# Kernel tuning notes

Hardware: AMD Instinct MI355X
Metric: run time of the kernel (lower is better)

Reference implementation:

```python
import jax, jax.numpy as jnp
import numpy as np

B, T, WSZ, HS = 32768, 168, 4, 1  # batch, seq (one week of hours), weather dims, HIDDEN_DIM


def _uniform(key, shape, lim):
    return jax.random.uniform(key, shape, jnp.float32, -lim, lim)


def setup_inputs() -> dict:
    key = jax.random.key(0)
    ks = jax.random.split(key, 12)
    stdv = 1.0 / np.sqrt(HS)  # pew_LSTM init: uniform(-1/sqrt(H), 1/sqrt(H))
    xav = np.sqrt(6.0 / (HS + 1))  # xavier_uniform for fc (in=HS, out=1)
    return {
        "input": jax.random.normal(ks[0], (B, T, WSZ + 1), dtype=jnp.float32),
        # pew_LSTM layer 1 (input_sz=1)
        "W1_ih": _uniform(ks[1], (1, 4 * HS), stdv),
        "W1_hh": _uniform(ks[2], (HS, 4 * HS), stdv),
        "W1_wh": _uniform(ks[3], (WSZ, 4 * HS), stdv),
        "b1": _uniform(ks[4], (4 * HS,), stdv),
        # pew_LSTM layer 2 (input_sz=HS)
        "W2_ih": _uniform(ks[5], (HS, 4 * HS), stdv),
        "W2_hh": _uniform(ks[6], (HS, 4 * HS), stdv),
        "W2_wh": _uniform(ks[7], (WSZ, 4 * HS), stdv),
        "b2": _uniform(ks[8], (4 * HS,), stdv),
        # final Linear(HS, 1)
        "fc_w": _uniform(ks[9], (1, HS), xav),
        "fc_b": jnp.zeros((1,), jnp.float32),
    }


def _pew_lstm(x, w, Wih, Whh, Wwh, b):
    """Custom LSTM with per-step weather input added to the gate pre-activations.
    x: [B,T,D_in], w: [B,T,WSZ] -> hidden_seq [B,T,HS], c_T [B,HS]."""
    bs = x.shape[0]
    h0 = jnp.zeros((bs, HS), x.dtype)
    c0 = jnp.zeros((bs, HS), x.dtype)
    # input- and weather-dependent gate terms are time-parallel; precompute once
    g_pre = jnp.einsum('btd,dg->btg', x, Wih) + jnp.einsum('btw,wg->btg', w, Wwh) + b

    def step(carry, gp_t):
        h, c = carry
        gates = gp_t + h @ Whh  # [B, 4*HS]
        i = jax.nn.sigmoid(gates[:, 0 * HS:1 * HS])
        f = jax.nn.sigmoid(gates[:, 1 * HS:2 * HS])
        g = jnp.tanh(gates[:, 2 * HS:3 * HS])
        o = jax.nn.sigmoid(gates[:, 3 * HS:4 * HS])
        c = f * c + i * g
        h = o * jnp.tanh(c)
        return (h, c), h

    (_, cT), hs = jax.lax.scan(step, (h0, c0), jnp.swapaxes(g_pre, 0, 1))
    return jnp.swapaxes(hs, 0, 1), cT  # [B,T,HS], [B,HS]


def reference(input, W1_ih, W1_hh, W1_wh, b1, W2_ih, W2_hh, W2_wh, b2, fc_w, fc_b):
    x_weather = input[:, :, :-1]            # [B,T,4]
    x_input = input[:, :, -1:]              # [B,T,1]
    h1, _ = _pew_lstm(x_input, x_weather, W1_ih, W1_hh, W1_wh, b1)
    h2, _ = _pew_lstm(h1, x_weather, W2_ih, W2_hh, W2_wh, b2)
    out = h2.reshape(-1, HS) @ fc_w.T + fc_b  # [B*T, 1]
    return out.reshape(-1)                    # [B*T]
```

## Files before the change

kernel.cpp:

```cpp
#include <hip/hip_runtime.h>


constexpr int BB  = 32768;
constexpr int TT  = 168;
constexpr int CHS = 8;
constexpr int CHV = 10;
constexpr int NCH = 21;

#define LOG2E  1.44269504088896341f
#define NEG2L  (-2.88539008177792681f)
#define ACLAMP 40.0f

__device__ __forceinline__ float lane_swap(float x) {
    return __int_as_float(
        __builtin_amdgcn_mov_dpp(__float_as_int(x), 0xB1, 0xF, 0xF, true));
}

__global__ __launch_bounds__(64, 1) void pewlstm_kernel(
    const float* __restrict__ in,
    const float* __restrict__ W1ih, const float* __restrict__ W1hh,
    const float* __restrict__ W1wh, const float* __restrict__ b1,
    const float* __restrict__ W2ih, const float* __restrict__ W2hh,
    const float* __restrict__ W2wh, const float* __restrict__ b2,
    const float* __restrict__ fcw, const float* __restrict__ fcb,
    float* __restrict__ out)
{
    const int tid = blockIdx.x * 64 + threadIdx.x;
    const int b   = tid >> 1;
    const int l2  = tid & 1;
    const float l2f = l2 ? 1.0f : 0.0f;

    const float* Wih = l2 ? W2ih : W1ih;
    const float* Whh = l2 ? W2hh : W1hh;
    const float* Wwh = l2 ? W2wh : W1wh;
    const float* Bv  = l2 ? b2   : b1;

    float wih[4], whh[4], bbv[4], wwh[16];
#pragma unroll
    for (int g = 0; g < 4; ++g) {
        const float s = (g == 2) ? NEG2L : -LOG2E;
        wih[g] = Wih[g] * s; whh[g] = Whh[g] * s; bbv[g] = Bv[g] * s;
    }
#pragma unroll
    for (int k = 0; k < 16; ++k) {
        const float s = ((k & 3) == 2) ? NEG2L : -LOG2E;
        wwh[k] = Wwh[k] * s;
    }
    const float fw = fcw[0], fbv = fcb[0];

    const float4* __restrict__ row =
        reinterpret_cast<const float4*>(in + (size_t)b * (TT * 5));
    float4* orow = reinterpret_cast<float4*>(out + (size_t)b * TT);

    float4 pref[CHV];
#pragma unroll
    for (int i = 0; i < CHV; ++i) pref[i] = row[i];

    float h = 0.f, cc = 0.f, h1x = 0.f;
    float xc0 = 0.f, xc1 = 0.f, xc2 = 0.f, xc3 = 0.f;
    float ob[CHS];
    float preA[CHS][4], preB[CHS][4];
    float cur[CHS * 5];

    auto commit = [&]() {
#pragma unroll
        for (int i = 0; i < CHV; ++i) {
            float4 v = pref[i];
            cur[4*i+0] = v.x; cur[4*i+1] = v.y;
            cur[4*i+2] = v.z; cur[4*i+3] = v.w;
        }
    };
    auto issue = [&](int c2) {
        const float4* nr = row + c2 * CHV;
#pragma unroll
        for (int i = 0; i < CHV; ++i) pref[i] = nr[i];
    };

    auto run_chunk = [&](float (&pC)[CHS][4], float (&pN)[CHS][4],
                         int c, bool buildNext) {
        const bool is0 = (c == 0);
#pragma unroll
        for (int s = 0; s < CHS; ++s) {
            if (buildNext) {
                const float w0 = l2 ? (s == 0 ? xc0 : cur[(s-1)*5+0]) : cur[s*5+0];
                const float w1 = l2 ? (s == 0 ? xc1 : cur[(s-1)*5+1]) : cur[s*5+1];
                const float w2 = l2 ? (s == 0 ? xc2 : cur[(s-1)*5+2]) : cur[s*5+2];
                const float w3 = l2 ? (s == 0 ? xc3 : cur[(s-1)*5+3]) : cur[s*5+3];
                const float xi = l2 ? 0.0f : cur[s*5+4];
#pragma unroll
                for (int g = 0; g < 4; ++g) {
                    float p = bbv[g];
                    p = fmaf(w0, wwh[0  + g], p);
                    p = fmaf(w1, wwh[4  + g], p);
                    p = fmaf(w2, wwh[8  + g], p);
                    p = fmaf(w3, wwh[12 + g], p);
                    pN[s][g] = fmaf(xi, wih[g], p);
                }
            }
            const float inv = h1x * l2f;
            float a0 = fmaf(h, whh[0], fmaf(inv, wih[0], pC[s][0]));
            float a1 = fmaf(h, whh[1], fmaf(inv, wih[1], pC[s][1]));
            float a2 = fmaf(h, whh[2], fmaf(inv, wih[2], pC[s][2]));
            float a3 = fmaf(h, whh[3], fmaf(inv, wih[3], pC[s][3]));
            a0 = fminf(a0, ACLAMP); a1 = fminf(a1, ACLAMP);
            a2 = fminf(a2, ACLAMP); a3 = fminf(a3, ACLAMP);
            const float eI = __builtin_amdgcn_exp2f(a0);
            const float eF = __builtin_amdgcn_exp2f(a1);
            const float eG = __builtin_amdgcn_exp2f(a2);
            const float eO = __builtin_amdgcn_exp2f(a3);
            const float dI = 1.f + eI, dF = 1.f + eF;
            const float dG = 1.f + eG, dO = 1.f + eO;
            const float nG = 1.f - eG;
            const float p   = dI * dG;
            const float num = fmaf(cc, p, nG * dF);
            const float den = dF * p;
            cc = num * __builtin_amdgcn_rcpf(den);
            const float Cm = fminf(cc * NEG2L, ACLAMP);
            const float eC = __builtin_amdgcn_exp2f(Cm);
            const float dC = 1.f + eC, nC = 1.f - eC;
            h = nC * __builtin_amdgcn_rcpf(dO * dC);

            if (s == 0) { if (is0 && l2) { h = 0.f; cc = 0.f; } }

            ob[(s + CHS - 1) & (CHS - 1)] = fmaf(h, fw, fbv);

            if (s == 0 && l2 && c >= 1) {
                orow[(c-1)*2+0] = make_float4(ob[0], ob[1], ob[2], ob[3]);
                orow[(c-1)*2+1] = make_float4(ob[4], ob[5], ob[6], ob[7]);
            }

            h1x = lane_swap(h);
        }
        if (buildNext) {
            xc0 = cur[35]; xc1 = cur[36]; xc2 = cur[37]; xc3 = cur[38];
        }
    };

    commit();
#pragma unroll
    for (int s = 0; s < CHS; ++s) {
        const float w0 = l2 ? (s == 0 ? 0.f : cur[(s-1)*5+0]) : cur[s*5+0];
        const float w1 = l2 ? (s == 0 ? 0.f : cur[(s-1)*5+1]) : cur[s*5+1];
        const float w2 = l2 ? (s == 0 ? 0.f : cur[(s-1)*5+2]) : cur[s*5+2];
        const float w3 = l2 ? (s == 0 ? 0.f : cur[(s-1)*5+3]) : cur[s*5+3];
        const float xi = l2 ? 0.0f : cur[s*5+4];
#pragma unroll
        for (int g = 0; g < 4; ++g) {
            float pp = bbv[g];
            pp = fmaf(w0, wwh[0  + g], pp);
            pp = fmaf(w1, wwh[4  + g], pp);
            pp = fmaf(w2, wwh[8  + g], pp);
            pp = fmaf(w3, wwh[12 + g], pp);
            preA[s][g] = fmaf(xi, wih[g], pp);
        }
    }
    xc0 = cur[35]; xc1 = cur[36]; xc2 = cur[37]; xc3 = cur[38];
    issue(1);

    for (int cp = 0; cp < 10; ++cp) {
        const int c0 = 2 * cp;
        commit();
        if (c0 + 2 < NCH) issue(c0 + 2);
        run_chunk(preA, preB, c0, true);

        commit();
        if (c0 + 3 < NCH) issue(c0 + 3);
        run_chunk(preB, preA, c0 + 1, true);
    }

    run_chunk(preA, preB, NCH - 1, false);

    {
        float a[4];
#pragma unroll
        for (int g = 0; g < 4; ++g) {
            float pp = bbv[g];
            pp = fmaf(xc0, wwh[0  + g], pp);
            pp = fmaf(xc1, wwh[4  + g], pp);
            pp = fmaf(xc2, wwh[8  + g], pp);
            pp = fmaf(xc3, wwh[12 + g], pp);
            pp = fmaf(h1x, wih[g], pp);
            a[g] = fminf(fmaf(h, whh[g], pp), ACLAMP);
        }
        const float eI = __builtin_amdgcn_exp2f(a[0]);
        const float eF = __builtin_amdgcn_exp2f(a[1]);
        const float eG = __builtin_amdgcn_exp2f(a[2]);
        const float eO = __builtin_amdgcn_exp2f(a[3]);
        const float dI = 1.f + eI, dF = 1.f + eF;
        const float dG = 1.f + eG, dO = 1.f + eO;
        const float nG = 1.f - eG;
        const float p   = dI * dG;
        const float num = fmaf(cc, p, nG * dF);
        cc = num * __builtin_amdgcn_rcpf(dF * p);
        const float Cm = fminf(cc * NEG2L, ACLAMP);
        const float eC = __builtin_amdgcn_exp2f(Cm);
        h = (1.f - eC) * __builtin_amdgcn_rcpf(dO * (1.f + eC));
        ob[7] = fmaf(h, fw, fbv);
        if (l2) {
            orow[(NCH-1)*2+0] = make_float4(ob[0], ob[1], ob[2], ob[3]);
            orow[(NCH-1)*2+1] = make_float4(ob[4], ob[5], ob[6], ob[7]);
        }
    }
}

extern "C" void kernel_launch(void* const* d_in, const int* in_sizes, int n_in,
                              void* d_out, int out_size, void* d_ws, size_t ws_size,
                              hipStream_t stream) {
    const float* in   = (const float*)d_in[0];
    const float* W1ih = (const float*)d_in[1];
    const float* W1hh = (const float*)d_in[2];
    const float* W1wh = (const float*)d_in[3];
    const float* b1   = (const float*)d_in[4];
    const float* W2ih = (const float*)d_in[5];
    const float* W2hh = (const float*)d_in[6];
    const float* W2wh = (const float*)d_in[7];
    const float* b2   = (const float*)d_in[8];
    const float* fcw  = (const float*)d_in[9];
    const float* fcb  = (const float*)d_in[10];
    float* out = (float*)d_out;

    pewlstm_kernel<<<(BB * 2) / 64, 64, 0, stream>>>(
        in, W1ih, W1hh, W1wh, b1, W2ih, W2hh, W2wh, b2, fcw, fcb, out);
}
```

Measured before the change: 33.39 us.

## Split LSTM gates across lane pairs with DPP exchange, four lanes per batch row

Each batch row is now handled by four lanes instead of two: per layer, two lanes each compute two of the four gate pre-activations and exponentials, then exchange denominators through DPP moves. Hidden state is broadcast back with DPP so both lanes of a layer carry the same h and c. This halves the per-lane exp and FMA work on the serial recurrence chain and doubles the number of waves in flight, with launch bounds raised accordingly. In exchange each lane adds three DPP moves per step, and the weather stream is loaded redundantly by four lanes per row.

```diff
diff --git a/kernel.cpp b/kernel.cpp
--- a/kernel.cpp
+++ b/kernel.cpp
@@ -11,12 +11,17 @@
 #define NEG2L  (-2.88539008177792681f)
 #define ACLAMP 40.0f
 
-__device__ __forceinline__ float lane_swap(float x) {
-    return __int_as_float(
-        __builtin_amdgcn_mov_dpp(__float_as_int(x), 0xB1, 0xF, 0xF, true));
-}
-
-__global__ __launch_bounds__(64, 1) void pewlstm_kernel(
+__device__ __forceinline__ float dpp_pull(float x) {
+    return __int_as_float(__builtin_amdgcn_mov_dpp(__float_as_int(x), 0xB1, 0xF, 0xF, true));
+}
+__device__ __forceinline__ float dpp_bA(float x) {
+    return __int_as_float(__builtin_amdgcn_mov_dpp(__float_as_int(x), 0xA0, 0xF, 0xF, true));
+}
+__device__ __forceinline__ float dpp_b0(float x) {
+    return __int_as_float(__builtin_amdgcn_mov_dpp(__float_as_int(x), 0x00, 0xF, 0xF, true));
+}
+
+__global__ __launch_bounds__(64, 2) void pewlstm_kernel(
     const float* __restrict__ in,
     const float* __restrict__ W1ih, const float* __restrict__ W1hh,
     const float* __restrict__ W1wh, const float* __restrict__ b1,
@@ -26,8 +31,10 @@
     float* __restrict__ out)
 {
     const int tid = blockIdx.x * 64 + threadIdx.x;
-    const int b   = tid >> 1;
-    const int l2  = tid & 1;
+    const int q   = tid >> 2;
+    const int r   = tid & 3;
+    const int l2  = r >> 1;
+    const int go  = (r & 1) * 2;
     const float l2f = l2 ? 1.0f : 0.0f;
 
     const float* Wih = l2 ? W2ih : W1ih;
@@ -35,22 +42,22 @@
     const float* Wwh = l2 ? W2wh : W1wh;
     const float* Bv  = l2 ? b2   : b1;
 
-    float wih[4], whh[4], bbv[4], wwh[16];
-#pragma unroll
-    for (int g = 0; g < 4; ++g) {
-        const float s = (g == 2) ? NEG2L : -LOG2E;
-        wih[g] = Wih[g] * s; whh[g] = Whh[g] * s; bbv[g] = Bv[g] * s;
-    }
-#pragma unroll
-    for (int k = 0; k < 16; ++k) {
-        const float s = ((k & 3) == 2) ? NEG2L : -LOG2E;
-        wwh[k] = Wwh[k] * s;
+    const float sLo = (go == 2) ? NEG2L : -LOG2E;
+    const float sHi = -LOG2E;
+    const float wihLo = Wih[go] * sLo,  wihHi = Wih[go + 1] * sHi;
+    const float whhLo = Whh[go] * sLo,  whhHi = Whh[go + 1] * sHi;
+    const float bLo   = Bv[go]  * sLo,  bHi   = Bv[go + 1]  * sHi;
+    float wwLo[4], wwHi[4];
+#pragma unroll
+    for (int w = 0; w < 4; ++w) {
+        wwLo[w] = Wwh[w * 4 + go]     * sLo;
+        wwHi[w] = Wwh[w * 4 + go + 1] * sHi;
     }
     const float fw = fcw[0], fbv = fcb[0];
 
     const float4* __restrict__ row =
-        reinterpret_cast<const float4*>(in + (size_t)b * (TT * 5));
-    float4* orow = reinterpret_cast<float4*>(out + (size_t)b * TT);
+        reinterpret_cast<const float4*>(in + (size_t)q * (TT * 5));
+    float4* orow = reinterpret_cast<float4*>(out + (size_t)q * TT);
 
     float4 pref[CHV];
 #pragma unroll
@@ -59,7 +66,7 @@
     float h = 0.f, cc = 0.f, h1x = 0.f;
     float xc0 = 0.f, xc1 = 0.f, xc2 = 0.f, xc3 = 0.f;
     float ob[CHS];
-    float preA[CHS][4], preB[CHS][4];
+    float pLoA[CHS], pHiA[CHS], pLoB[CHS], pHiB[CHS];
     float cur[CHS * 5];
 
     auto commit = [&]() {
@@ -76,127 +83,106 @@
         for (int i = 0; i < CHV; ++i) pref[i] = nr[i];
     };
 
-    auto run_chunk = [&](float (&pC)[CHS][4], float (&pN)[CHS][4],
-                         int c, bool buildNext) {
-        const bool is0 = (c == 0);
+    auto build = [&](float (&pLo)[CHS], float (&pHi)[CHS]) {
 #pragma unroll
         for (int s = 0; s < CHS; ++s) {
-            if (buildNext) {
-                const float w0 = l2 ? (s == 0 ? xc0 : cur[(s-1)*5+0]) : cur[s*5+0];
-                const float w1 = l2 ? (s == 0 ? xc1 : cur[(s-1)*5+1]) : cur[s*5+1];
-                const float w2 = l2 ? (s == 0 ? xc2 : cur[(s-1)*5+2]) : cur[s*5+2];
-                const float w3 = l2 ? (s == 0 ? xc3 : cur[(s-1)*5+3]) : cur[s*5+3];
-                const float xi = l2 ? 0.0f : cur[s*5+4];
-#pragma unroll
-                for (int g = 0; g < 4; ++g) {
-                    float p = bbv[g];
-                    p = fmaf(w0, wwh[0  + g], p);
-                    p = fmaf(w1, wwh[4  + g], p);
-                    p = fmaf(w2, wwh[8  + g], p);
-                    p = fmaf(w3, wwh[12 + g], p);
-                    pN[s][g] = fmaf(xi, wih[g], p);
-                }
-            }
+            const float w0 = l2 ? (s == 0 ? xc0 : cur[(s-1)*5+0]) : cur[s*5+0];
+            const float w1 = l2 ? (s == 0 ? xc1 : cur[(s-1)*5+1]) : cur[s*5+1];
+            const float w2 = l2 ? (s == 0 ? xc2 : cur[(s-1)*5+2]) : cur[s*5+2];
+            const float w3 = l2 ? (s == 0 ? xc3 : cur[(s-1)*5+3]) : cur[s*5+3];
+            const float xi = l2 ? 0.0f : cur[s*5+4];
+            float a = bLo;
+            a = fmaf(w0, wwLo[0], a); a = fmaf(w1, wwLo[1], a);
+            a = fmaf(w2, wwLo[2], a); a = fmaf(w3, wwLo[3], a);
+            pLo[s] = fmaf(xi, wihLo, a);
+            float bb = bHi;
+            bb = fmaf(w0, wwHi[0], bb); bb = fmaf(w1, wwHi[1], bb);
+            bb = fmaf(w2, wwHi[2], bb); bb = fmaf(w3, wwHi[3], bb);
+            pHi[s] = fmaf(xi, wihHi, bb);
+        }
+        xc0 = cur[35]; xc1 = cur[36]; xc2 = cur[37]; xc3 = cur[38];
+    };
+
+    auto phase2 = [&](float (&pLo)[CHS], float (&pHi)[CHS], int c, bool is0) {
+#pragma unroll
+        for (int s = 0; s < CHS; ++s) {
             const float inv = h1x * l2f;
-            float a0 = fmaf(h, whh[0], fmaf(inv, wih[0], pC[s][0]));
-            float a1 = fmaf(h, whh[1], fmaf(inv, wih[1], pC[s][1]));
-            float a2 = fmaf(h, whh[2], fmaf(inv, wih[2], pC[s][2]));
-            float a3 = fmaf(h, whh[3], fmaf(inv, wih[3], pC[s][3]));
-            a0 = fminf(a0, ACLAMP); a1 = fminf(a1, ACLAMP);
-            a2 = fminf(a2, ACLAMP); a3 = fminf(a3, ACLAMP);
-            const float eI = __builtin_amdgcn_exp2f(a0);
-            const float eF = __builtin_amdgcn_exp2f(a1);
-            const float eG = __builtin_amdgcn_exp2f(a2);
-            const float eO = __builtin_amdgcn_exp2f(a3);
-            const float dI = 1.f + eI, dF = 1.f + eF;
-            const float dG = 1.f + eG, dO = 1.f + eO;
-            const float nG = 1.f - eG;
-            const float p   = dI * dG;
-            const float num = fmaf(cc, p, nG * dF);
-            const float den = dF * p;
+            float aLo = fmaf(h, whhLo, fmaf(inv, wihLo, pLo[s]));
+            float aHi = fmaf(h, whhHi, fmaf(inv, wihHi, pHi[s]));
+            aLo = fminf(aLo, ACLAMP); aHi = fminf(aHi, ACLAMP);
+            const float eLo = __builtin_amdgcn_exp2f(aLo);
+            const float eHi = __builtin_amdgcn_exp2f(aHi);
+            const float dLo = 1.f + eLo;
+            const float dHi = 1.f + eHi;
+            const float nLo = 1.f - eLo;
+            const float dG = dpp_pull(dLo);
+            const float nG = dpp_pull(nLo);
+            const float dO = dpp_pull(dHi);
+            const float p   = dLo * dG;
+            const float num = fmaf(cc, p, nG * dHi);
+            const float den = dHi * p;
             cc = num * __builtin_amdgcn_rcpf(den);
             const float Cm = fminf(cc * NEG2L, ACLAMP);
             const float eC = __builtin_amdgcn_exp2f(Cm);
-            const float dC = 1.f + eC, nC = 1.f - eC;
-            h = nC * __builtin_amdgcn_rcpf(dO * dC);
-
-            if (s == 0) { if (is0 && l2) { h = 0.f; cc = 0.f; } }
-
-            ob[(s + CHS - 1) & (CHS - 1)] = fmaf(h, fw, fbv);
-
-            if (s == 0 && l2 && c >= 1) {
+            h = (1.f - eC) * __builtin_amdgcn_rcpf(dO * (1.f + eC));
+
+            if (s == 0 && is0) { if (l2) { h = 0.f; cc = 0.f; } }
+
+            ob[(s + 7) & 7] = fmaf(h, fw, fbv);
+
+            if (s == 0 && c >= 1 && r == 2) {
                 orow[(c-1)*2+0] = make_float4(ob[0], ob[1], ob[2], ob[3]);
                 orow[(c-1)*2+1] = make_float4(ob[4], ob[5], ob[6], ob[7]);
             }
 
-            h1x = lane_swap(h);
-        }
-        if (buildNext) {
-            xc0 = cur[35]; xc1 = cur[36]; xc2 = cur[37]; xc3 = cur[38];
+            const float hb = h;
+            h1x = dpp_b0(hb);
+            h   = dpp_bA(hb);
         }
     };
 
     commit();
-#pragma unroll
-    for (int s = 0; s < CHS; ++s) {
-        const float w0 = l2 ? (s == 0 ? 0.f : cur[(s-1)*5+0]) : cur[s*5+0];
-        const float w1 = l2 ? (s == 0 ? 0.f : cur[(s-1)*5+1]) : cur[s*5+1];
-        const float w2 = l2 ? (s == 0 ? 0.f : cur[(s-1)*5+2]) : cur[s*5+2];
-        const float w3 = l2 ? (s == 0 ? 0.f : cur[(s-1)*5+3]) : cur[s*5+3];
-        const float xi = l2 ? 0.0f : cur[s*5+4];
-#pragma unroll
-        for (int g = 0; g < 4; ++g) {
-            float pp = bbv[g];
-            pp = fmaf(w0, wwh[0  + g], pp);
-            pp = fmaf(w1, wwh[4  + g], pp);
-            pp = fmaf(w2, wwh[8  + g], pp);
-            pp = fmaf(w3, wwh[12 + g], pp);
-            preA[s][g] = fmaf(xi, wih[g], pp);
-        }
-    }
-    xc0 = cur[35]; xc1 = cur[36]; xc2 = cur[37]; xc3 = cur[38];
+    build(pLoA, pHiA);
     issue(1);
 
     for (int cp = 0; cp < 10; ++cp) {
         const int c0 = 2 * cp;
         commit();
         if (c0 + 2 < NCH) issue(c0 + 2);
-        run_chunk(preA, preB, c0, true);
+        build(pLoB, pHiB);
+        phase2(pLoA, pHiA, c0, c0 == 0);
 
         commit();
         if (c0 + 3 < NCH) issue(c0 + 3);
-        run_chunk(preB, preA, c0 + 1, true);
+        build(pLoA, pHiA);
+        phase2(pLoB, pHiB, c0 + 1, false);
     }
 
-    run_chunk(preA, preB, NCH - 1, false);
+    phase2(pLoA, pHiA, NCH - 1, false);
 
     {
-        float a[4];
-#pragma unroll
-        for (int g = 0; g < 4; ++g) {
-            float pp = bbv[g];
-            pp = fmaf(xc0, wwh[0  + g], pp);
-            pp = fmaf(xc1, wwh[4  + g], pp);
-            pp = fmaf(xc2, wwh[8  + g], pp);
-            pp = fmaf(xc3, wwh[12 + g], pp);
-            pp = fmaf(h1x, wih[g], pp);
-            a[g] = fminf(fmaf(h, whh[g], pp), ACLAMP);
-        }
-        const float eI = __builtin_amdgcn_exp2f(a[0]);
-        const float eF = __builtin_amdgcn_exp2f(a[1]);
-        const float eG = __builtin_amdgcn_exp2f(a[2]);
-        const float eO = __builtin_amdgcn_exp2f(a[3]);
-        const float dI = 1.f + eI, dF = 1.f + eF;
-        const float dG = 1.f + eG, dO = 1.f + eO;
-        const float nG = 1.f - eG;
-        const float p   = dI * dG;
-        const float num = fmaf(cc, p, nG * dF);
-        cc = num * __builtin_amdgcn_rcpf(dF * p);
+        float aLo = bLo, aHi = bHi;
+        aLo = fmaf(xc0, wwLo[0], aLo); aHi = fmaf(xc0, wwHi[0], aHi);
+        aLo = fmaf(xc1, wwLo[1], aLo); aHi = fmaf(xc1, wwHi[1], aHi);
+        aLo = fmaf(xc2, wwLo[2], aLo); aHi = fmaf(xc2, wwHi[2], aHi);
+        aLo = fmaf(xc3, wwLo[3], aLo); aHi = fmaf(xc3, wwHi[3], aHi);
+        aLo = fmaf(h1x, wihLo, aLo);   aHi = fmaf(h1x, wihHi, aHi);
+        aLo = fmaf(h,   whhLo, aLo);   aHi = fmaf(h,   whhHi, aHi);
+        aLo = fminf(aLo, ACLAMP); aHi = fminf(aHi, ACLAMP);
+        const float eLo = __builtin_amdgcn_exp2f(aLo);
+        const float eHi = __builtin_amdgcn_exp2f(aHi);
+        const float dLo = 1.f + eLo, dHi = 1.f + eHi, nLo = 1.f - eLo;
+        const float dG = dpp_pull(dLo);
+        const float nG = dpp_pull(nLo);
+        const float dO = dpp_pull(dHi);
+        const float p   = dLo * dG;
+        const float num = fmaf(cc, p, nG * dHi);
+        cc = num * __builtin_amdgcn_rcpf(dHi * p);
         const float Cm = fminf(cc * NEG2L, ACLAMP);
         const float eC = __builtin_amdgcn_exp2f(Cm);
         h = (1.f - eC) * __builtin_amdgcn_rcpf(dO * (1.f + eC));
         ob[7] = fmaf(h, fw, fbv);
-        if (l2) {
+        if (r == 2) {
             orow[(NCH-1)*2+0] = make_float4(ob[0], ob[1], ob[2], ob[3]);
             orow[(NCH-1)*2+1] = make_float4(ob[4], ob[5], ob[6], ob[7]);
         }
@@ -219,6 +205,6 @@
     const float* fcb  = (const float*)d_in[10];
     float* out = (float*)d_out;
 
-    pewlstm_kernel<<<(BB * 2) / 64, 64, 0, stream>>>(
+    pewlstm_kernel<<<(BB * 4) / 64, 64, 0, stream>>>(
         in, W1ih, W1hh, W1wh, b1, W2ih, W2hh, W2wh, b2, fcw, fcb, out);
 }
```

New measurement: 90.06 us. +169.8%, slower.

## Replace hardware exp2/rcp with polynomial and Newton software versions, inline gate precompute

Applied to the files above, without the earlier changes.

Swaps the hardware exp2 and reciprocal intrinsics for a degree-6 polynomial exp2 with exponent bit construction and a three-step Newton reciprocal built from FMAs. The aim is to move work off the quarter-rate transcendental unit onto full-rate FMA pipes. It also drops the double-buffered gate pre-activation arrays in favour of computing the weather/input terms inline per step, with raw input double-buffered instead, and clamps only the h-independent part of the pre-activation. This adds many instructions and a longer dependent chain per recurrent step, and changes numerical behaviour at extreme inputs.

```diff
diff --git a/kernel.cpp b/kernel.cpp
--- a/kernel.cpp
+++ b/kernel.cpp
@@ -7,13 +7,39 @@
 constexpr int CHV = 10;
 constexpr int NCH = 21;
 
-#define LOG2E  1.44269504088896341f
-#define NEG2L  (-2.88539008177792681f)
-#define ACLAMP 40.0f
+#define LOG2E   1.44269504088896341f
+#define NEG2L   (-2.88539008177792681f)
+#define A0CLAMP 37.0f
 
 __device__ __forceinline__ float lane_swap(float x) {
     return __int_as_float(
         __builtin_amdgcn_mov_dpp(__float_as_int(x), 0xB1, 0xF, 0xF, true));
+}
+
+__device__ __forceinline__ float exp2_soft(float x) {
+    float n  = floorf(x);
+    float f  = x - n;
+    float nc = fminf(fmaxf(n, -126.0f), 60.0f);
+    int   ni = (int)nc;
+    float scale = __int_as_float((ni + 127) << 23);
+    float f2  = f * f;
+    float p01 = fmaf(f, 0.6931471805599453f,    1.0f);
+    float p23 = fmaf(f, 0.05550410866482158f,   0.2402265069591007f);
+    float p45 = fmaf(f, 0.0013333558146428443f, 0.009618129107628477f);
+    float inn = fmaf(f2, 0.00015403530393381606f, p45);
+    float f4  = f2 * f2;
+    float t1  = fmaf(f2, p23, p01);
+    float t2  = fmaf(f4, inn, t1);
+    return t2 * scale;
+}
+
+__device__ __forceinline__ float rcp_soft(float x) {
+    float y = __int_as_float(0x7EF311C3 - __float_as_int(x));
+    float e;
+    e = fmaf(-x, y, 1.0f); y = fmaf(y, e, y);
+    e = fmaf(-x, y, 1.0f); y = fmaf(y, e, y);
+    e = fmaf(-x, y, 1.0f); y = fmaf(y, e, y);
+    return y;
 }
 
 __global__ __launch_bounds__(64, 1) void pewlstm_kernel(
@@ -52,123 +78,83 @@
         reinterpret_cast<const float4*>(in + (size_t)b * (TT * 5));
     float4* orow = reinterpret_cast<float4*>(out + (size_t)b * TT);
 
-    float4 pref[CHV];
-#pragma unroll
-    for (int i = 0; i < CHV; ++i) pref[i] = row[i];
-
+    float4 bufA[CHV], bufB[CHV];
     float h = 0.f, cc = 0.f, h1x = 0.f;
     float xc0 = 0.f, xc1 = 0.f, xc2 = 0.f, xc3 = 0.f;
     float ob[CHS];
-    float preA[CHS][4], preB[CHS][4];
-    float cur[CHS * 5];
-
-    auto commit = [&]() {
+
+    auto issue = [&](float4 (&buf)[CHV], int c2) {
+#pragma unroll
+        for (int i = 0; i < CHV; ++i) buf[i] = row[c2 * CHV + i];
+    };
+
+    auto process = [&](float4 (&buf)[CHV], int c, bool is0) {
+        float cur[CHS * 5];
 #pragma unroll
         for (int i = 0; i < CHV; ++i) {
-            float4 v = pref[i];
-            cur[4*i+0] = v.x; cur[4*i+1] = v.y;
-            cur[4*i+2] = v.z; cur[4*i+3] = v.w;
-        }
-    };
-    auto issue = [&](int c2) {
-        const float4* nr = row + c2 * CHV;
-#pragma unroll
-        for (int i = 0; i < CHV; ++i) pref[i] = nr[i];
-    };
-
-    auto run_chunk = [&](float (&pC)[CHS][4], float (&pN)[CHS][4],
-                         int c, bool buildNext) {
-        const bool is0 = (c == 0);
+            cur[4*i+0] = buf[i].x; cur[4*i+1] = buf[i].y;
+            cur[4*i+2] = buf[i].z; cur[4*i+3] = buf[i].w;
+        }
 #pragma unroll
         for (int s = 0; s < CHS; ++s) {
-            if (buildNext) {
-                const float w0 = l2 ? (s == 0 ? xc0 : cur[(s-1)*5+0]) : cur[s*5+0];
-                const float w1 = l2 ? (s == 0 ? xc1 : cur[(s-1)*5+1]) : cur[s*5+1];
-                const float w2 = l2 ? (s == 0 ? xc2 : cur[(s-1)*5+2]) : cur[s*5+2];
-                const float w3 = l2 ? (s == 0 ? xc3 : cur[(s-1)*5+3]) : cur[s*5+3];
-                const float xi = l2 ? 0.0f : cur[s*5+4];
-#pragma unroll
-                for (int g = 0; g < 4; ++g) {
-                    float p = bbv[g];
-                    p = fmaf(w0, wwh[0  + g], p);
-                    p = fmaf(w1, wwh[4  + g], p);
-                    p = fmaf(w2, wwh[8  + g], p);
-                    p = fmaf(w3, wwh[12 + g], p);
-                    pN[s][g] = fmaf(xi, wih[g], p);
-                }
+            const float w0 = l2 ? (s == 0 ? xc0 : cur[(s-1)*5+0]) : cur[s*5+0];
+            const float w1 = l2 ? (s == 0 ? xc1 : cur[(s-1)*5+1]) : cur[s*5+1];
+            const float w2 = l2 ? (s == 0 ? xc2 : cur[(s-1)*5+2]) : cur[s*5+2];
+            const float w3 = l2 ? (s == 0 ? xc3 : cur[(s-1)*5+3]) : cur[s*5+3];
+            const float xi = l2 ? 0.0f : cur[s*5+4];
+
+            float a0[4];
+#pragma unroll
+            for (int g = 0; g < 4; ++g) {
+                float p = bbv[g];
+                p = fmaf(w0, wwh[0  + g], p);
+                p = fmaf(w1, wwh[4  + g], p);
+                p = fmaf(w2, wwh[8  + g], p);
+                p = fmaf(w3, wwh[12 + g], p);
+                p = fmaf(xi, wih[g], p);
+                a0[g] = fminf(p, A0CLAMP);
             }
+
             const float inv = h1x * l2f;
-            float a0 = fmaf(h, whh[0], fmaf(inv, wih[0], pC[s][0]));
-            float a1 = fmaf(h, whh[1], fmaf(inv, wih[1], pC[s][1]));
-            float a2 = fmaf(h, whh[2], fmaf(inv, wih[2], pC[s][2]));
-            float a3 = fmaf(h, whh[3], fmaf(inv, wih[3], pC[s][3]));
-            a0 = fminf(a0, ACLAMP); a1 = fminf(a1, ACLAMP);
-            a2 = fminf(a2, ACLAMP); a3 = fminf(a3, ACLAMP);
-            const float eI = __builtin_amdgcn_exp2f(a0);
-            const float eF = __builtin_amdgcn_exp2f(a1);
-            const float eG = __builtin_amdgcn_exp2f(a2);
-            const float eO = __builtin_amdgcn_exp2f(a3);
+            const float aI = fmaf(h, whh[0], fmaf(inv, wih[0], a0[0]));
+            const float aF = fmaf(h, whh[1], fmaf(inv, wih[1], a0[1]));
+            const float aG = fmaf(h, whh[2], fmaf(inv, wih[2], a0[2]));
+            const float aO = fmaf(h, whh[3], fmaf(inv, wih[3], a0[3]));
+            const float eI = exp2_soft(aI);
+            const float eF = exp2_soft(aF);
+            const float eG = exp2_soft(aG);
+            const float eO = exp2_soft(aO);
             const float dI = 1.f + eI, dF = 1.f + eF;
             const float dG = 1.f + eG, dO = 1.f + eO;
             const float nG = 1.f - eG;
             const float p   = dI * dG;
             const float num = fmaf(cc, p, nG * dF);
-            const float den = dF * p;
-            cc = num * __builtin_amdgcn_rcpf(den);
-            const float Cm = fminf(cc * NEG2L, ACLAMP);
-            const float eC = __builtin_amdgcn_exp2f(Cm);
-            const float dC = 1.f + eC, nC = 1.f - eC;
-            h = nC * __builtin_amdgcn_rcpf(dO * dC);
-
-            if (s == 0) { if (is0 && l2) { h = 0.f; cc = 0.f; } }
-
-            ob[(s + CHS - 1) & (CHS - 1)] = fmaf(h, fw, fbv);
-
-            if (s == 0 && l2 && c >= 1) {
+            cc = num * rcp_soft(dF * p);
+            const float eC = exp2_soft(cc * NEG2L);
+            h = (1.f - eC) * rcp_soft(dO * (1.f + eC));
+
+            if (s == 0 && is0) { if (l2) { h = 0.f; cc = 0.f; } }
+
+            ob[(s + 7) & 7] = fmaf(h, fw, fbv);
+
+            if (s == 0 && c >= 1 && l2) {
                 orow[(c-1)*2+0] = make_float4(ob[0], ob[1], ob[2], ob[3]);
                 orow[(c-1)*2+1] = make_float4(ob[4], ob[5], ob[6], ob[7]);
             }
 
             h1x = lane_swap(h);
         }
-        if (buildNext) {
-            xc0 = cur[35]; xc1 = cur[36]; xc2 = cur[37]; xc3 = cur[38];
-        }
+        xc0 = cur[35]; xc1 = cur[36]; xc2 = cur[37]; xc3 = cur[38];
     };
 
-    commit();
-#pragma unroll
-    for (int s = 0; s < CHS; ++s) {
-        const float w0 = l2 ? (s == 0 ? 0.f : cur[(s-1)*5+0]) : cur[s*5+0];
-        const float w1 = l2 ? (s == 0 ? 0.f : cur[(s-1)*5+1]) : cur[s*5+1];
-        const float w2 = l2 ? (s == 0 ? 0.f : cur[(s-1)*5+2]) : cur[s*5+2];
-        const float w3 = l2 ? (s == 0 ? 0.f : cur[(s-1)*5+3]) : cur[s*5+3];
-        const float xi = l2 ? 0.0f : cur[s*5+4];
-#pragma unroll
-        for (int g = 0; g < 4; ++g) {
-            float pp = bbv[g];
-            pp = fmaf(w0, wwh[0  + g], pp);
-            pp = fmaf(w1, wwh[4  + g], pp);
-            pp = fmaf(w2, wwh[8  + g], pp);
-            pp = fmaf(w3, wwh[12 + g], pp);
-            preA[s][g] = fmaf(xi, wih[g], pp);
-        }
-    }
-    xc0 = cur[35]; xc1 = cur[36]; xc2 = cur[37]; xc3 = cur[38];
-    issue(1);
-
+    issue(bufA, 0);
     for (int cp = 0; cp < 10; ++cp) {
-        const int c0 = 2 * cp;
-        commit();
-        if (c0 + 2 < NCH) issue(c0 + 2);
-        run_chunk(preA, preB, c0, true);
-
-        commit();
-        if (c0 + 3 < NCH) issue(c0 + 3);
-        run_chunk(preB, preA, c0 + 1, true);
-    }
-
-    run_chunk(preA, preB, NCH - 1, false);
+        issue(bufB, 2 * cp + 1);
+        process(bufA, 2 * cp, cp == 0);
+        issue(bufA, 2 * cp + 2);
+        process(bufB, 2 * cp + 1, false);
+    }
+    process(bufA, 20, false);
 
     {
         float a[4];
@@ -179,22 +165,22 @@
             pp = fmaf(xc1, wwh[4  + g], pp);
             pp = fmaf(xc2, wwh[8  + g], pp);
             pp = fmaf(xc3, wwh[12 + g], pp);
+            pp = fminf(pp, A0CLAMP);
             pp = fmaf(h1x, wih[g], pp);
-            a[g] = fminf(fmaf(h, whh[g], pp), ACLAMP);
-        }
-        const float eI = __builtin_amdgcn_exp2f(a[0]);
-        const float eF = __builtin_amdgcn_exp2f(a[1]);
-        const float eG = __builtin_amdgcn_exp2f(a[2]);
-        const float eO = __builtin_amdgcn_exp2f(a[3]);
+            a[g] = fmaf(h, whh[g], pp);
+        }
+        const float eI = exp2_soft(a[0]);
+        const float eF = exp2_soft(a[1]);
+        const float eG = exp2_soft(a[2]);
+        const float eO = exp2_soft(a[3]);
         const float dI = 1.f + eI, dF = 1.f + eF;
         const float dG = 1.f + eG, dO = 1.f + eO;
         const float nG = 1.f - eG;
         const float p   = dI * dG;
         const float num = fmaf(cc, p, nG * dF);
-        cc = num * __builtin_amdgcn_rcpf(dF * p);
-        const float Cm = fminf(cc * NEG2L, ACLAMP);
-        const float eC = __builtin_amdgcn_exp2f(Cm);
-        h = (1.f - eC) * __builtin_amdgcn_rcpf(dO * (1.f + eC));
+        cc = num * rcp_soft(dF * p);
+        const float eC = exp2_soft(cc * NEG2L);
+        h = (1.f - eC) * rcp_soft(dO * (1.f + eC));
         ob[7] = fmaf(h, fw, fbv);
         if (l2) {
             orow[(NCH-1)*2+0] = make_float4(ob[0], ob[1], ob[2], ob[3]);
```

New measurement: 50.02 us. 1.5x slower.

## Replace transcendental rcp/exp for cell path with ALU polynomial and serialize build phase

Applied to the files above, without the earlier changes.

Swaps the hardware rcp and exp2 on the cell-state tanh and the cell and hidden updates for software versions: Newton-Raphson reciprocal and a polynomial exp2. This is meant to move work off the transcendental unit onto FMA ALUs. It also drops the double-buffered pre-activation arrays, so each chunk's recurrence runs first and the next chunk's gate precompute follows, instead of being interleaved with it. That costs more VALU instructions per step and gives up overlap between independent precompute and the serial recurrence chain.

```diff
diff --git a/kernel.cpp b/kernel.cpp
--- a/kernel.cpp
+++ b/kernel.cpp
@@ -14,6 +14,29 @@
 __device__ __forceinline__ float lane_swap(float x) {
     return __int_as_float(
         __builtin_amdgcn_mov_dpp(__float_as_int(x), 0xB1, 0xF, 0xF, true));
+}
+
+__device__ __forceinline__ float rcp2(float x) {
+    float y = __int_as_float(0x7EF311C3 - __float_as_int(x));
+    float e;
+    e = fmaf(-x, y, 1.0f); y = fmaf(y, e, y);
+    e = fmaf(-x, y, 1.0f); y = fmaf(y, e, y);
+    return y;
+}
+
+__device__ __forceinline__ float exp2s(float x) {
+    float n  = floorf(x);
+    float f  = x - n;
+    float scale = __int_as_float(((int)n + 127) << 23);
+    float f2  = f * f;
+    float p01 = fmaf(f, 0.6931471805599453f,    1.0f);
+    float p23 = fmaf(f, 0.05550410866482158f,   0.2402265069591007f);
+    float p45 = fmaf(f, 0.0013333558146428443f, 0.009618129107628477f);
+    float inn = fmaf(f2, 0.00015403530393381606f, p45);
+    float f4  = f2 * f2;
+    float t1  = fmaf(f2, p23, p01);
+    float t2  = fmaf(f4, inn, t1);
+    return t2 * scale;
 }
 
 __global__ __launch_bounds__(64, 1) void pewlstm_kernel(
@@ -59,7 +82,7 @@
     float h = 0.f, cc = 0.f, h1x = 0.f;
     float xc0 = 0.f, xc1 = 0.f, xc2 = 0.f, xc3 = 0.f;
     float ob[CHS];
-    float preA[CHS][4], preB[CHS][4];
+    float pre[CHS][4];
     float cur[CHS * 5];
 
     auto commit = [&]() {
@@ -75,33 +98,35 @@
 #pragma unroll
         for (int i = 0; i < CHV; ++i) pref[i] = nr[i];
     };
-
-    auto run_chunk = [&](float (&pC)[CHS][4], float (&pN)[CHS][4],
-                         int c, bool buildNext) {
-        const bool is0 = (c == 0);
+    auto build = [&]() {
 #pragma unroll
         for (int s = 0; s < CHS; ++s) {
-            if (buildNext) {
-                const float w0 = l2 ? (s == 0 ? xc0 : cur[(s-1)*5+0]) : cur[s*5+0];
-                const float w1 = l2 ? (s == 0 ? xc1 : cur[(s-1)*5+1]) : cur[s*5+1];
-                const float w2 = l2 ? (s == 0 ? xc2 : cur[(s-1)*5+2]) : cur[s*5+2];
-                const float w3 = l2 ? (s == 0 ? xc3 : cur[(s-1)*5+3]) : cur[s*5+3];
-                const float xi = l2 ? 0.0f : cur[s*5+4];
-#pragma unroll
-                for (int g = 0; g < 4; ++g) {
-                    float p = bbv[g];
-                    p = fmaf(w0, wwh[0  + g], p);
-                    p = fmaf(w1, wwh[4  + g], p);
-                    p = fmaf(w2, wwh[8  + g], p);
-                    p = fmaf(w3, wwh[12 + g], p);
-                    pN[s][g] = fmaf(xi, wih[g], p);
-                }
+            const float w0 = l2 ? (s == 0 ? xc0 : cur[(s-1)*5+0]) : cur[s*5+0];
+            const float w1 = l2 ? (s == 0 ? xc1 : cur[(s-1)*5+1]) : cur[s*5+1];
+            const float w2 = l2 ? (s == 0 ? xc2 : cur[(s-1)*5+2]) : cur[s*5+2];
+            const float w3 = l2 ? (s == 0 ? xc3 : cur[(s-1)*5+3]) : cur[s*5+3];
+            const float xi = l2 ? 0.0f : cur[s*5+4];
+#pragma unroll
+            for (int g = 0; g < 4; ++g) {
+                float p = bbv[g];
+                p = fmaf(w0, wwh[0  + g], p);
+                p = fmaf(w1, wwh[4  + g], p);
+                p = fmaf(w2, wwh[8  + g], p);
+                p = fmaf(w3, wwh[12 + g], p);
+                pre[s][g] = fmaf(xi, wih[g], p);
             }
+        }
+        xc0 = cur[35]; xc1 = cur[36]; xc2 = cur[37]; xc3 = cur[38];
+    };
+
+    auto phase2 = [&](int c, bool is0) {
+#pragma unroll
+        for (int s = 0; s < CHS; ++s) {
             const float inv = h1x * l2f;
-            float a0 = fmaf(h, whh[0], fmaf(inv, wih[0], pC[s][0]));
-            float a1 = fmaf(h, whh[1], fmaf(inv, wih[1], pC[s][1]));
-            float a2 = fmaf(h, whh[2], fmaf(inv, wih[2], pC[s][2]));
-            float a3 = fmaf(h, whh[3], fmaf(inv, wih[3], pC[s][3]));
+            float a0 = fmaf(h, whh[0], fmaf(inv, wih[0], pre[s][0]));
+            float a1 = fmaf(h, whh[1], fmaf(inv, wih[1], pre[s][1]));
+            float a2 = fmaf(h, whh[2], fmaf(inv, wih[2], pre[s][2]));
+            float a3 = fmaf(h, whh[3], fmaf(inv, wih[3], pre[s][3]));
             a0 = fminf(a0, ACLAMP); a1 = fminf(a1, ACLAMP);
             a2 = fminf(a2, ACLAMP); a3 = fminf(a3, ACLAMP);
             const float eI = __builtin_amdgcn_exp2f(a0);
@@ -113,62 +138,36 @@
             const float nG = 1.f - eG;
             const float p   = dI * dG;
             const float num = fmaf(cc, p, nG * dF);
-            const float den = dF * p;
-            cc = num * __builtin_amdgcn_rcpf(den);
-            const float Cm = fminf(cc * NEG2L, ACLAMP);
-            const float eC = __builtin_amdgcn_exp2f(Cm);
-            const float dC = 1.f + eC, nC = 1.f - eC;
-            h = nC * __builtin_amdgcn_rcpf(dO * dC);
-
-            if (s == 0) { if (is0 && l2) { h = 0.f; cc = 0.f; } }
-
-            ob[(s + CHS - 1) & (CHS - 1)] = fmaf(h, fw, fbv);
-
-            if (s == 0 && l2 && c >= 1) {
+            cc = num * rcp2(dF * p);
+            float Cm = cc * NEG2L;
+            Cm = fminf(fmaxf(Cm, -43.0f), 43.0f);
+            const float eC = exp2s(Cm);
+            h = (1.f - eC) * rcp2(dO * (1.f + eC));
+
+            if (s == 0 && is0) { if (l2) { h = 0.f; cc = 0.f; } }
+
+            ob[(s + 7) & 7] = fmaf(h, fw, fbv);
+
+            if (s == 0 && c >= 1 && l2) {
                 orow[(c-1)*2+0] = make_float4(ob[0], ob[1], ob[2], ob[3]);
                 orow[(c-1)*2+1] = make_float4(ob[4], ob[5], ob[6], ob[7]);
             }
 
             h1x = lane_swap(h);
         }
-        if (buildNext) {
-            xc0 = cur[35]; xc1 = cur[36]; xc2 = cur[37]; xc3 = cur[38];
-        }
     };
 
     commit();
-#pragma unroll
-    for (int s = 0; s < CHS; ++s) {
-        const float w0 = l2 ? (s == 0 ? 0.f : cur[(s-1)*5+0]) : cur[s*5+0];
-        const float w1 = l2 ? (s == 0 ? 0.f : cur[(s-1)*5+1]) : cur[s*5+1];
-        const float w2 = l2 ? (s == 0 ? 0.f : cur[(s-1)*5+2]) : cur[s*5+2];
-        const float w3 = l2 ? (s == 0 ? 0.f : cur[(s-1)*5+3]) : cur[s*5+3];
-        const float xi = l2 ? 0.0f : cur[s*5+4];
-#pragma unroll
-        for (int g = 0; g < 4; ++g) {
-            float pp = bbv[g];
-            pp = fmaf(w0, wwh[0  + g], pp);
-            pp = fmaf(w1, wwh[4  + g], pp);
-            pp = fmaf(w2, wwh[8  + g], pp);
-            pp = fmaf(w3, wwh[12 + g], pp);
-            preA[s][g] = fmaf(xi, wih[g], pp);
-        }
-    }
-    xc0 = cur[35]; xc1 = cur[36]; xc2 = cur[37]; xc3 = cur[38];
+    build();
     issue(1);
 
-    for (int cp = 0; cp < 10; ++cp) {
-        const int c0 = 2 * cp;
+    for (int c = 0; c < NCH - 1; ++c) {
+        phase2(c, c == 0);
         commit();
-        if (c0 + 2 < NCH) issue(c0 + 2);
-        run_chunk(preA, preB, c0, true);
-
-        commit();
-        if (c0 + 3 < NCH) issue(c0 + 3);
-        run_chunk(preB, preA, c0 + 1, true);
-    }
-
-    run_chunk(preA, preB, NCH - 1, false);
+        if (c + 2 < NCH) issue(c + 2);
+        build();
+    }
+    phase2(NCH - 1, false);
 
     {
         float a[4];
@@ -191,10 +190,11 @@
         const float nG = 1.f - eG;
         const float p   = dI * dG;
         const float num = fmaf(cc, p, nG * dF);
-        cc = num * __builtin_amdgcn_rcpf(dF * p);
-        const float Cm = fminf(cc * NEG2L, ACLAMP);
-        const float eC = __builtin_amdgcn_exp2f(Cm);
-        h = (1.f - eC) * __builtin_amdgcn_rcpf(dO * (1.f + eC));
+        cc = num * rcp2(dF * p);
+        float Cm = cc * NEG2L;
+        Cm = fminf(fmaxf(Cm, -43.0f), 43.0f);
+        const float eC = exp2s(Cm);
+        h = (1.f - eC) * rcp2(dO * (1.f + eC));
         ob[7] = fmaf(h, fw, fbv);
         if (l2) {
             orow[(NCH-1)*2+0] = make_float4(ob[0], ob[1], ob[2], ob[3]);
```

After: 47.42 us. 1.42x slower.
